# Kernel optimization log

Measured on AMD Instinct MI355X. Metric: run time of the kernel, lower is better.

The kernel has to match this reference:

```python
import jax, jax.numpy as jnp
import numpy as np

ANCHORS = jnp.array([[1.3221, 1.73145], [3.19275, 4.00944], [5.05587, 8.09892],
                     [9.47112, 4.84053], [11.2364, 10.0071]], dtype=jnp.float32)
NUM_ANCHORS = 5
NUM_CLASSES = 20
MAX_BOXES = 50
NOOBJECT_SCALE = 1.0
OBJECT_SCALE = 5.0
COORD_SCALE = 1.0
CLASS_SCALE = 1.0
SIL_THRESH = 0.6


def iou_cwh(b1, b2):
    # boxes as (cx, cy, w, h); matches repo bbox_ious(x1y1x2y2=False)
    x1, y1, w1, h1 = b1[..., 0], b1[..., 1], b1[..., 2], b1[..., 3]
    x2, y2, w2, h2 = b2[..., 0], b2[..., 1], b2[..., 2], b2[..., 3]
    uw = jnp.maximum(x1 + w1 * 0.5, x2 + w2 * 0.5) - jnp.minimum(x1 - w1 * 0.5, x2 - w2 * 0.5)
    uh = jnp.maximum(y1 + h1 * 0.5, y2 + h2 * 0.5) - jnp.minimum(y1 - h1 * 0.5, y2 - h2 * 0.5)
    cw = w1 + w2 - uw
    ch = h1 + h2 - uh
    inter = jnp.where((cw <= 0) | (ch <= 0), 0.0, cw * ch)
    return inter / (w1 * h1 + w2 * h2 - inter)


def setup_inputs() -> dict:
    key = jax.random.key(0)
    k1, k2, k3, k4 = jax.random.split(key, 4)
    nB = 64
    output = jax.random.normal(k1, (nB, NUM_ANCHORS * (5 + NUM_CLASSES), 38, 38), dtype=jnp.float32)
    # target layout per box: (class, x, y, w, h), all normalized; x>0 marks a valid box
    cls_col = jax.random.randint(k2, (nB, MAX_BOXES, 1), 0, NUM_CLASSES).astype(jnp.float32)
    xy = jax.random.uniform(k3, (nB, MAX_BOXES, 2), minval=0.05, maxval=0.95)
    wh = jax.random.uniform(k4, (nB, MAX_BOXES, 2), minval=0.02, maxval=0.3)
    target = jnp.concatenate([cls_col, xy, wh], axis=-1).reshape(nB, MAX_BOXES * 5)
    return {"output": output, "target": target}


def region_loss(output, target):
    nB = output.shape[0]
    nA, nC = NUM_ANCHORS, NUM_CLASSES
    nH, nW = output.shape[2], output.shape[3]
    out = output.reshape(nB, nA, 5 + nC, nH, nW)
    x = jax.nn.sigmoid(out[:, :, 0])
    y = jax.nn.sigmoid(out[:, :, 1])
    w = out[:, :, 2]
    h = out[:, :, 3]
    conf = jax.nn.sigmoid(out[:, :, 4])
    # [nB,nA,nC,nH,nW] -> [nB*nA*nH*nW, nC] (matches torch transpose/view order)
    cls_logits = jnp.transpose(out[:, :, 5:], (0, 1, 3, 4, 2)).reshape(-1, nC)

    sg = jax.lax.stop_gradient
    aw, ah = ANCHORS[:, 0], ANCHORS[:, 1]
    grid_x = jnp.arange(nW, dtype=jnp.float32)[None, None, None, :]
    grid_y = jnp.arange(nH, dtype=jnp.float32)[None, None, :, None]
    px = sg(x) + grid_x
    py = sg(y) + grid_y
    pw = jnp.exp(sg(w)) * aw[None, :, None, None]
    ph = jnp.exp(sg(h)) * ah[None, :, None, None]
    pred_boxes = jnp.stack([px, py, pw, ph], axis=-1)  # [nB,nA,nH,nW,4]

    # ---- build_targets (vectorized) ----
    tgt = sg(target).reshape(nB, MAX_BOXES, 5)
    gcls = tgt[:, :, 0]
    gx = tgt[:, :, 1] * nW
    gy = tgt[:, :, 2] * nH
    gw = tgt[:, :, 3] * nW
    gh = tgt[:, :, 4] * nH
    # loop breaks at first x==0 -> cumulative validity
    valid = jnp.cumprod((tgt[:, :, 1] != 0).astype(jnp.int32), axis=1).astype(bool)

    # silence conf_mask where any-GT IoU > thresh
    pb_flat = pred_boxes.reshape(nB, nA * nH * nW, 4)
    gt_boxes = jnp.stack([gx, gy, gw, gh], axis=-1)  # [nB,50,4]
    ious = iou_cwh(pb_flat[:, :, None, :], gt_boxes[:, None, :, :])  # [nB,nAnc,50]
    ious = jnp.where(valid[:, None, :], ious, 0.0)
    max_iou = jnp.max(ious, axis=2)
    conf_mask = jnp.where(max_iou > SIL_THRESH, 0.0, NOOBJECT_SCALE).reshape(nB, nA, nH, nW)

    # seen < 12800 defaults
    shp = (nB, nA, nH, nW)
    coord_mask = jnp.ones(shp, jnp.float32)
    tx = jnp.full(shp, 0.5, jnp.float32)
    ty = jnp.full(shp, 0.5, jnp.float32)
    tw = jnp.zeros(shp, jnp.float32)
    th = jnp.zeros(shp, jnp.float32)
    tconf = jnp.zeros(shp, jnp.float32)
    tcls = jnp.zeros(shp, jnp.float32)
    cls_mask = jnp.zeros(shp, jnp.float32)

    # best anchor per GT by (0,0,w,h) IoU; argmax keeps first max like the strict '>' loop
    zA = jnp.zeros_like(aw)
    anchor_boxes = jnp.stack([zA, zA, aw, ah], axis=-1)  # [nA,4]
    zg = jnp.zeros_like(gw)
    gt_wh = jnp.stack([zg, zg, gw, gh], axis=-1)  # [nB,50,4]
    a_iou = iou_cwh(gt_wh[:, :, None, :], anchor_boxes[None, None, :, :])  # [nB,50,nA]
    best_n = jnp.argmax(a_iou, axis=2)  # [nB,50]

    gi = jnp.clip(gx.astype(jnp.int32), 0, nW - 1)
    gj = jnp.clip(gy.astype(jnp.int32), 0, nH - 1)
    aw_b = aw[best_n]
    ah_b = ah[best_n]
    tx_v = gx - gi.astype(jnp.float32)
    ty_v = gy - gj.astype(jnp.float32)
    tw_v = jnp.log(gw / aw_b)
    th_v = jnp.log(gh / ah_b)
    b_ix = jnp.arange(nB)
    pred_at = pred_boxes[b_ix[:, None], best_n, gj, gi]  # [nB,50,4]
    iou_gt = iou_cwh(gt_boxes, pred_at)  # [nB,50]

    def step(carry, t):
        cm, clm, tx_, ty_, tw_, th_, tcf, tcl = carry
        bsel = jnp.where(valid[:, t], b_ix, nB)  # out-of-bounds -> dropped
        n, j, i = best_n[:, t], gj[:, t], gi[:, t]
        st = lambda a, v: a.at[bsel, n, j, i].set(v, mode='drop')
        cm = st(cm, jnp.full((nB,), OBJECT_SCALE, jnp.float32))
        clm = st(clm, jnp.ones((nB,), jnp.float32))
        tx_ = st(tx_, tx_v[:, t])
        ty_ = st(ty_, ty_v[:, t])
        tw_ = st(tw_, tw_v[:, t])
        th_ = st(th_, th_v[:, t])
        tcf = st(tcf, iou_gt[:, t])
        tcl = st(tcl, gcls[:, t])
        return (cm, clm, tx_, ty_, tw_, th_, tcf, tcl), None

    init = (conf_mask, cls_mask, tx, ty, tw, th, tconf, tcls)
    (conf_mask, cls_mask, tx, ty, tw, th, tconf, tcls), _ = jax.lax.scan(
        step, init, jnp.arange(MAX_BOXES))

    # ---- losses ----
    cmf = jnp.sqrt(conf_mask)
    loss_x = COORD_SCALE * jnp.sum((x * coord_mask - tx * coord_mask) ** 2) / 2.0
    loss_y = COORD_SCALE * jnp.sum((y * coord_mask - ty * coord_mask) ** 2) / 2.0
    loss_w = COORD_SCALE * jnp.sum((w * coord_mask - tw * coord_mask) ** 2) / 2.0
    loss_h = COORD_SCALE * jnp.sum((h * coord_mask - th * coord_mask) ** 2) / 2.0
    loss_conf = jnp.sum((conf * cmf - tconf * cmf) ** 2) / 2.0
    logp = jax.nn.log_softmax(cls_logits, axis=-1)
    labels = tcls.reshape(-1).astype(jnp.int32)
    ce = -jnp.take_along_axis(logp, labels[:, None], axis=1)[:, 0]
    loss_cls = CLASS_SCALE * jnp.sum(ce * cls_mask.reshape(-1))
    return loss_x + loss_y + loss_w + loss_h + loss_conf + loss_cls


def reference(output, target):
    return region_loss(output, target)
```

## Files before the change

kernel.cpp:

```cpp
#include <hip/hip_runtime.h>
#include <math.h>

#define NA 5
#define NC 20
#define NH 38
#define NW 38
#define MAX_BOXES 50
#define SPAT (NH * NW)
#define CELLS_PER_B (NA * SPAT)
#define CPB 1024
#define OBJECT_SCALE 5.0f
#define NOOBJECT_SCALE 1.0f

__constant__ float c_aw[NA] = {1.3221f, 3.19275f, 5.05587f, 9.47112f, 11.2364f};
__constant__ float c_ah[NA] = {1.73145f, 4.00944f, 8.09892f, 4.84053f, 10.0071f};

__device__ __forceinline__ float sigmoidf_(float v) { return 1.f / (1.f + expf(-v)); }

__device__ __forceinline__ float iou_cwh8(float x1, float y1, float w1, float h1,
                                          float x2, float y2, float w2, float h2) {
  float uw = fmaxf(x1 + w1 * 0.5f, x2 + w2 * 0.5f) - fminf(x1 - w1 * 0.5f, x2 - w2 * 0.5f);
  float uh = fmaxf(y1 + h1 * 0.5f, y2 + h2 * 0.5f) - fminf(y1 - h1 * 0.5f, y2 - h2 * 0.5f);
  float cw = w1 + w2 - uw;
  float ch = h1 + h2 - uh;
  float inter = (cw <= 0.f || ch <= 0.f) ? 0.f : cw * ch;
  return inter / (w1 * h1 + w2 * h2 - inter);
}

__global__ __launch_bounds__(256) void region_loss_kernel(
    const float* __restrict__ out, const float* __restrict__ target,
    float* __restrict__ outv) {
  const int b = blockIdx.y;
  const int s0 = blockIdx.x * CPB;
  const int tid = threadIdx.x;

  __shared__ float4 sb_lo[MAX_BOXES];
  __shared__ float  sb_ag[MAX_BOXES];
  __shared__ int s_wcnt;
  __shared__ int s_wcell[MAX_BOXES];
  __shared__ float s_wdata[MAX_BOXES][6];
  __shared__ float s_red[4];

  int sC[4];
  bool ok[4];
  const float* basep[4];
  float v0[4], v1[4], v2[4], v3[4], v4[4];
  float fi[4], fj[4], paw[4], pah[4];
#pragma unroll
  for (int q = 0; q < 4; ++q) {
    int s = s0 + (q << 8) + tid;
    ok[q] = (s < CELLS_PER_B);
    int sc = ok[q] ? s : 0;
    sC[q] = ok[q] ? s : -1;
    unsigned a = (unsigned)sc / SPAT;
    unsigned r = (unsigned)sc - a * SPAT;
    unsigned j = r / NW, i = r - j * NW;
    fi[q] = (float)i; fj[q] = (float)j;
    paw[q] = c_aw[a]; pah[q] = c_ah[a];
    const float* bp = out + ((size_t)(b * NA + a) * 25) * SPAT + r;
    basep[q] = bp;
    v0[q] = bp[0];
    v1[q] = bp[SPAT];
    v2[q] = bp[2 * SPAT];
    v3[q] = bp[3 * SPAT];
    v4[q] = bp[4 * SPAT];
  }

  if (tid == 64) s_wcnt = 0;
  __syncthreads();

  if (tid < 64) {
    int t = tid;
    float cls = 0.f, x = 0.f, y = 0.f, w = 0.f, h = 0.f;
    if (t < MAX_BOXES) {
      const float* tg = target + (size_t)(b * MAX_BOXES + t) * 5;
      cls = tg[0]; x = tg[1]; y = tg[2]; w = tg[3]; h = tg[4];
    }
    unsigned long long nz = __ballot(t < MAX_BOXES && x != 0.f);
    unsigned long long low = (t < 63) ? ((1ull << (t + 1)) - 1ull) : ~0ull;
    bool valid = (t < MAX_BOXES) && ((nz & low) == low);

    float gx = x * NW, gy = y * NH, gw = w * NW, gh = h * NH;

    int best = 0; float bestiou = -1.f;
#pragma unroll
    for (int a2 = 0; a2 < NA; ++a2) {
      float aiou = iou_cwh8(0.f, 0.f, gw, gh, 0.f, 0.f, c_aw[a2], c_ah[a2]);
      if (aiou > bestiou) { bestiou = aiou; best = a2; }
    }
    int gi = min(max((int)gx, 0), NW - 1);
    int gj = min(max((int)gy, 0), NH - 1);

    const float* pb = out + ((size_t)(b * NA + best) * 25) * SPAT + gj * NW + gi;
    float px = sigmoidf_(pb[0]) + (float)gi;
    float py = sigmoidf_(pb[SPAT]) + (float)gj;
    float pw2 = expf(pb[2 * SPAT]) * c_aw[best];
    float ph2 = expf(pb[3 * SPAT]) * c_ah[best];
    float iou_gt = iou_cwh8(gx, gy, gw, gh, px, py, pw2, ph2);

    int cell = best * SPAT + gj * NW + gi;
    unsigned long long vm = __ballot(valid);
    bool winner = valid;
    for (int tp = 0; tp < MAX_BOXES; ++tp) {
      int c2 = __shfl(cell, tp);
      if (tp > t && ((vm >> tp) & 1ull) && c2 == cell) winner = false;
    }

    if (t < MAX_BOXES) {
      if (valid) {
        sb_lo[t] = make_float4(gx - gw * 0.5f, gx + gw * 0.5f,
                               gy - gh * 0.5f, gy + gh * 0.5f);
        sb_ag[t] = 0.375f * (gw * gh);
      } else {
        sb_lo[t] = make_float4(1e30f, 1e30f, 1e30f, 1e30f);
        sb_ag[t] = 0.f;
      }
      if (winner && cell >= s0 && cell < s0 + CPB) {
        int k = atomicAdd(&s_wcnt, 1);
        s_wcell[k] = cell;
        s_wdata[k][0] = gx - (float)gi;
        s_wdata[k][1] = gy - (float)gj;
        s_wdata[k][2] = logf(gw / c_aw[best]);
        s_wdata[k][3] = logf(gh / c_ah[best]);
        s_wdata[k][4] = iou_gt;
        s_wdata[k][5] = cls;
      }
    }
  }
  __syncthreads();

  float xs[4], ys[4], cs[4], plx[4], phx[4], ply[4], phy[4], ap[4];
#pragma unroll
  for (int q = 0; q < 4; ++q) {
    xs[q] = sigmoidf_(v0[q]);
    ys[q] = sigmoidf_(v1[q]);
    cs[q] = sigmoidf_(v4[q]);
    float pw = expf(v2[q]) * paw[q], ph = expf(v3[q]) * pah[q];
    float px = xs[q] + fi[q], py = ys[q] + fj[q];
    plx[q] = px - pw * 0.5f; phx[q] = px + pw * 0.5f;
    ply[q] = py - ph * 0.5f; phy[q] = py + ph * 0.5f;
    ap[q] = 0.375f * (pw * ph);
  }

  bool sup[4] = {false, false, false, false};
#pragma unroll 5
  for (int t = 0; t < MAX_BOXES; ++t) {
    float4 lo = sb_lo[t];
    float ag = sb_ag[t];
#pragma unroll
    for (int q = 0; q < 4; ++q) {
      float cw = fminf(phx[q], lo.y) - fmaxf(plx[q], lo.x);
      float ch = fminf(phy[q], lo.w) - fmaxf(ply[q], lo.z);
      cw = fmaxf(cw, 0.f);
      ch = fmaxf(ch, 0.f);
      sup[q] = sup[q] | (cw * ch > ag + ap[q]);
    }
  }

  int cnt = s_wcnt;
  float acc = 0.f;
#pragma unroll
  for (int q = 0; q < 4; ++q) {
    if (!ok[q]) continue;
    float cmask = sup[q] ? 0.f : NOOBJECT_SCALE;
    float tx = 0.5f, ty = 0.5f, tw = 0.f, th = 0.f, tconf = 0.f, clsloss = 0.f;
    for (int k = 0; k < cnt; ++k) {
      if (s_wcell[k] == sC[q]) {
        cmask = OBJECT_SCALE;
        tx = s_wdata[k][0]; ty = s_wdata[k][1];
        tw = s_wdata[k][2]; th = s_wdata[k][3];
        tconf = s_wdata[k][4];
        int label = (int)s_wdata[k][5];
        const float* cb = basep[q] + 5 * SPAT;
        float m = -1e30f, lv = 0.f;
        for (int c = 0; c < NC; ++c) {
          float vv = cb[c * SPAT];
          if (c == label) lv = vv;
          m = fmaxf(m, vv);
        }
        float ssum = 0.f;
        for (int c = 0; c < NC; ++c) ssum += expf(cb[c * SPAT] - m);
        clsloss = (m + logf(ssum)) - lv;
      }
    }
    float dx = xs[q] - tx, dy = ys[q] - ty, dw = v2[q] - tw, dh = v3[q] - th;
    float dc = cs[q] - tconf;
    acc += 0.5f * (dx * dx + dy * dy + dw * dw + dh * dh + cmask * (dc * dc)) + clsloss;
  }

  for (int o = 32; o > 0; o >>= 1) acc += __shfl_down(acc, o, 64);
  int wid = tid >> 6, lane = tid & 63;
  if (lane == 0) s_red[wid] = acc;
  __syncthreads();
  if (tid == 0)
    atomicAdd(outv, s_red[0] + s_red[1] + s_red[2] + s_red[3]);
}

extern "C" void kernel_launch(void* const* d_in, const int* in_sizes, int n_in,
                              void* d_out, int out_size, void* d_ws, size_t ws_size,
                              hipStream_t stream) {
  const float* out = (const float*)d_in[0];
  const float* target = (const float*)d_in[1];
  int nB = in_sizes[0] / (NA * (5 + NC) * SPAT);
  int gx = (CELLS_PER_B + CPB - 1) / CPB;
  hipLaunchKernelGGL(region_loss_kernel, dim3(gx, nB), dim3(256), 0, stream,
                     out, target, (float*)d_out);
}
```

Baseline: 107.1 us.

## Shrink blocks to 128 threads, use fast intrinsics, max-reduce suppression test

Block size drops from 256 to 128 threads with 4 cells per thread, so each block covers 512 cells and the grid roughly doubles, giving more blocks to spread over the CUs. The hot-path sigmoid/exp/log calls become __expf/__logf/rcp intrinsics, and the anchor divisions become multiplies by reciprocals. The 50-box suppression test now keeps a running max of (inter - 0.375*area_gt) per cell and compares it once against the predicted-area term, replacing the per-box boolean OR. Fast intrinsics can change results near the IoU threshold, and the extra blocks mean more redundant per-block target setup.

```diff
diff --git a/kernel.cpp b/kernel.cpp
--- a/kernel.cpp
+++ b/kernel.cpp
@@ -8,26 +8,42 @@
 #define MAX_BOXES 50
 #define SPAT (NH * NW)
 #define CELLS_PER_B (NA * SPAT)
-#define CPB 1024
+#define TPB 128
+#define CELLS_PER_T 4
+#define CPB (TPB * CELLS_PER_T)
 #define OBJECT_SCALE 5.0f
 #define NOOBJECT_SCALE 1.0f
 
-__constant__ float c_aw[NA] = {1.3221f, 3.19275f, 5.05587f, 9.47112f, 11.2364f};
-__constant__ float c_ah[NA] = {1.73145f, 4.00944f, 8.09892f, 4.84053f, 10.0071f};
-
-__device__ __forceinline__ float sigmoidf_(float v) { return 1.f / (1.f + expf(-v)); }
-
-__device__ __forceinline__ float iou_cwh8(float x1, float y1, float w1, float h1,
+__constant__ float c_aw[NA]  = {1.3221f, 3.19275f, 5.05587f, 9.47112f, 11.2364f};
+__constant__ float c_ah[NA]  = {1.73145f, 4.00944f, 8.09892f, 4.84053f, 10.0071f};
+__constant__ float c_iaw[NA] = {1.f/1.3221f, 1.f/3.19275f, 1.f/5.05587f, 1.f/9.47112f, 1.f/11.2364f};
+__constant__ float c_iah[NA] = {1.f/1.73145f, 1.f/4.00944f, 1.f/8.09892f, 1.f/4.84053f, 1.f/10.0071f};
+
+__device__ __forceinline__ float fexp(float v) { return __expf(v); }
+__device__ __forceinline__ float flog(float v) { return __logf(v); }
+__device__ __forceinline__ float frcp(float v) { return __builtin_amdgcn_rcpf(v); }
+__device__ __forceinline__ float fsig(float v) { return frcp(1.f + __expf(-v)); }
+
+__device__ __forceinline__ float iou_fast(float x1, float y1, float w1, float h1,
                                           float x2, float y2, float w2, float h2) {
   float uw = fmaxf(x1 + w1 * 0.5f, x2 + w2 * 0.5f) - fminf(x1 - w1 * 0.5f, x2 - w2 * 0.5f);
   float uh = fmaxf(y1 + h1 * 0.5f, y2 + h2 * 0.5f) - fminf(y1 - h1 * 0.5f, y2 - h2 * 0.5f);
   float cw = w1 + w2 - uw;
   float ch = h1 + h2 - uh;
   float inter = (cw <= 0.f || ch <= 0.f) ? 0.f : cw * ch;
+  return inter * frcp(w1 * h1 + w2 * h2 - inter);
+}
+
+__device__ __forceinline__ float iou_wh_exact(float w1, float h1, float w2, float h2) {
+  float uw = fmaxf(w1 * 0.5f, w2 * 0.5f) - fminf(-w1 * 0.5f, -w2 * 0.5f);
+  float uh = fmaxf(h1 * 0.5f, h2 * 0.5f) - fminf(-h1 * 0.5f, -h2 * 0.5f);
+  float cw = w1 + w2 - uw;
+  float ch = h1 + h2 - uh;
+  float inter = (cw <= 0.f || ch <= 0.f) ? 0.f : cw * ch;
   return inter / (w1 * h1 + w2 * h2 - inter);
 }
 
-__global__ __launch_bounds__(256) void region_loss_kernel(
+__global__ __launch_bounds__(TPB) void region_loss_kernel(
     const float* __restrict__ out, const float* __restrict__ target,
     float* __restrict__ outv) {
   const int b = blockIdx.y;
@@ -39,16 +55,16 @@
   __shared__ int s_wcnt;
   __shared__ int s_wcell[MAX_BOXES];
   __shared__ float s_wdata[MAX_BOXES][6];
-  __shared__ float s_red[4];
-
-  int sC[4];
-  bool ok[4];
-  const float* basep[4];
-  float v0[4], v1[4], v2[4], v3[4], v4[4];
-  float fi[4], fj[4], paw[4], pah[4];
-#pragma unroll
-  for (int q = 0; q < 4; ++q) {
-    int s = s0 + (q << 8) + tid;
+  __shared__ float s_red[2];
+
+  int sC[CELLS_PER_T];
+  bool ok[CELLS_PER_T];
+  const float* basep[CELLS_PER_T];
+  float v0[CELLS_PER_T], v1[CELLS_PER_T], v2[CELLS_PER_T], v3[CELLS_PER_T], v4[CELLS_PER_T];
+  float fi[CELLS_PER_T], fj[CELLS_PER_T], paw[CELLS_PER_T], pah[CELLS_PER_T];
+#pragma unroll
+  for (int q = 0; q < CELLS_PER_T; ++q) {
+    int s = s0 + q * TPB + tid;
     ok[q] = (s < CELLS_PER_B);
     int sc = ok[q] ? s : 0;
     sC[q] = ok[q] ? s : -1;
@@ -66,7 +82,7 @@
     v4[q] = bp[4 * SPAT];
   }
 
-  if (tid == 64) s_wcnt = 0;
+  if (tid == TPB - 1) s_wcnt = 0;
   __syncthreads();
 
   if (tid < 64) {
@@ -85,18 +101,18 @@
     int best = 0; float bestiou = -1.f;
 #pragma unroll
     for (int a2 = 0; a2 < NA; ++a2) {
-      float aiou = iou_cwh8(0.f, 0.f, gw, gh, 0.f, 0.f, c_aw[a2], c_ah[a2]);
+      float aiou = iou_wh_exact(gw, gh, c_aw[a2], c_ah[a2]);
       if (aiou > bestiou) { bestiou = aiou; best = a2; }
     }
     int gi = min(max((int)gx, 0), NW - 1);
     int gj = min(max((int)gy, 0), NH - 1);
 
     const float* pb = out + ((size_t)(b * NA + best) * 25) * SPAT + gj * NW + gi;
-    float px = sigmoidf_(pb[0]) + (float)gi;
-    float py = sigmoidf_(pb[SPAT]) + (float)gj;
-    float pw2 = expf(pb[2 * SPAT]) * c_aw[best];
-    float ph2 = expf(pb[3 * SPAT]) * c_ah[best];
-    float iou_gt = iou_cwh8(gx, gy, gw, gh, px, py, pw2, ph2);
+    float px = fsig(pb[0]) + (float)gi;
+    float py = fsig(pb[SPAT]) + (float)gj;
+    float pw2 = fexp(pb[2 * SPAT]) * c_aw[best];
+    float ph2 = fexp(pb[3 * SPAT]) * c_ah[best];
+    float iou_gt = iou_fast(gx, gy, gw, gh, px, py, pw2, ph2);
 
     int cell = best * SPAT + gj * NW + gi;
     unsigned long long vm = __ballot(valid);
@@ -120,8 +136,8 @@
         s_wcell[k] = cell;
         s_wdata[k][0] = gx - (float)gi;
         s_wdata[k][1] = gy - (float)gj;
-        s_wdata[k][2] = logf(gw / c_aw[best]);
-        s_wdata[k][3] = logf(gh / c_ah[best]);
+        s_wdata[k][2] = flog(gw * c_iaw[best]);
+        s_wdata[k][3] = flog(gh * c_iah[best]);
         s_wdata[k][4] = iou_gt;
         s_wdata[k][5] = cls;
       }
@@ -129,40 +145,45 @@
   }
   __syncthreads();
 
-  float xs[4], ys[4], cs[4], plx[4], phx[4], ply[4], phy[4], ap[4];
-#pragma unroll
-  for (int q = 0; q < 4; ++q) {
-    xs[q] = sigmoidf_(v0[q]);
-    ys[q] = sigmoidf_(v1[q]);
-    cs[q] = sigmoidf_(v4[q]);
-    float pw = expf(v2[q]) * paw[q], ph = expf(v3[q]) * pah[q];
+  float xs[CELLS_PER_T], ys[CELLS_PER_T], cs[CELLS_PER_T];
+  float plx[CELLS_PER_T], phx[CELLS_PER_T], ply[CELLS_PER_T], phy[CELLS_PER_T];
+  float ap[CELLS_PER_T], msc[CELLS_PER_T];
+#pragma unroll
+  for (int q = 0; q < CELLS_PER_T; ++q) {
+    xs[q] = fsig(v0[q]);
+    ys[q] = fsig(v1[q]);
+    cs[q] = fsig(v4[q]);
+    float pw = fexp(v2[q]) * paw[q], ph = fexp(v3[q]) * pah[q];
     float px = xs[q] + fi[q], py = ys[q] + fj[q];
     plx[q] = px - pw * 0.5f; phx[q] = px + pw * 0.5f;
     ply[q] = py - ph * 0.5f; phy[q] = py + ph * 0.5f;
     ap[q] = 0.375f * (pw * ph);
-  }
-
-  bool sup[4] = {false, false, false, false};
-#pragma unroll 5
-  for (int t = 0; t < MAX_BOXES; ++t) {
-    float4 lo = sb_lo[t];
-    float ag = sb_ag[t];
-#pragma unroll
-    for (int q = 0; q < 4; ++q) {
-      float cw = fminf(phx[q], lo.y) - fmaxf(plx[q], lo.x);
-      float ch = fminf(phy[q], lo.w) - fmaxf(ply[q], lo.z);
-      cw = fmaxf(cw, 0.f);
-      ch = fmaxf(ch, 0.f);
-      sup[q] = sup[q] | (cw * ch > ag + ap[q]);
+    msc[q] = -1e30f;
+  }
+
+#pragma unroll
+  for (int c0 = 0; c0 < MAX_BOXES; c0 += 10) {
+    float4 bl[10]; float bag[10];
+#pragma unroll
+    for (int u = 0; u < 10; ++u) { bl[u] = sb_lo[c0 + u]; bag[u] = sb_ag[c0 + u]; }
+#pragma unroll
+    for (int u = 0; u < 10; ++u) {
+#pragma unroll
+      for (int q = 0; q < CELLS_PER_T; ++q) {
+        float cw = fminf(phx[q], bl[u].y) - fmaxf(plx[q], bl[u].x);
+        float ch = fminf(phy[q], bl[u].w) - fmaxf(ply[q], bl[u].z);
+        cw = fmaxf(cw, 0.f);
+        msc[q] = fmaxf(msc[q], fmaf(cw, ch, -bag[u]));
+      }
     }
   }
 
   int cnt = s_wcnt;
   float acc = 0.f;
 #pragma unroll
-  for (int q = 0; q < 4; ++q) {
+  for (int q = 0; q < CELLS_PER_T; ++q) {
     if (!ok[q]) continue;
-    float cmask = sup[q] ? 0.f : NOOBJECT_SCALE;
+    float cmask = (msc[q] > ap[q]) ? 0.f : NOOBJECT_SCALE;
     float tx = 0.5f, ty = 0.5f, tw = 0.f, th = 0.f, tconf = 0.f, clsloss = 0.f;
     for (int k = 0; k < cnt; ++k) {
       if (s_wcell[k] == sC[q]) {
@@ -179,8 +200,8 @@
           m = fmaxf(m, vv);
         }
         float ssum = 0.f;
-        for (int c = 0; c < NC; ++c) ssum += expf(cb[c * SPAT] - m);
-        clsloss = (m + logf(ssum)) - lv;
+        for (int c = 0; c < NC; ++c) ssum += fexp(cb[c * SPAT] - m);
+        clsloss = (m + flog(ssum)) - lv;
       }
     }
     float dx = xs[q] - tx, dy = ys[q] - ty, dw = v2[q] - tw, dh = v3[q] - th;
@@ -193,7 +214,7 @@
   if (lane == 0) s_red[wid] = acc;
   __syncthreads();
   if (tid == 0)
-    atomicAdd(outv, s_red[0] + s_red[1] + s_red[2] + s_red[3]);
+    atomicAdd(outv, s_red[0] + s_red[1]);
 }
 
 extern "C" void kernel_launch(void* const* d_in, const int* in_sizes, int n_in,
@@ -203,6 +224,6 @@
   const float* target = (const float*)d_in[1];
   int nB = in_sizes[0] / (NA * (5 + NC) * SPAT);
   int gx = (CELLS_PER_B + CPB - 1) / CPB;
-  hipLaunchKernelGGL(region_loss_kernel, dim3(gx, nB), dim3(256), 0, stream,
+  hipLaunchKernelGGL(region_loss_kernel, dim3(gx, nB), dim3(TPB), 0, stream,
                      out, target, (float*)d_out);
 }
```

Result: no change. 107.0 us (-0.1%).
